# Optimization experiments

Measured on AMD Instinct MI355X. Metric: run time of the kernel, lower is better.

Reference implementation:

```python
import jax, jax.numpy as jnp
import numpy as np
import math

B, C, H, W, T, NH, SS = 4, 64, 32, 32, 32, 8, 512


def _alibi_slopes(heads):
    def pow2(n):
        start = 2 ** (-2 ** (-(math.log2(n) - 3)))
        return [start * start ** i for i in range(n)]
    if math.log2(heads).is_integer():
        return pow2(heads)
    cp = 2 ** math.floor(math.log2(heads))
    return pow2(cp) + pow2(2 * cp)[0::2][: heads - cp]


def _style_conv(x, style, weight, lw, lb, noise_p, bias_p, noise):
    # x: (b,c,h,w,t); weight: (out,in,1,1,1) -> modulated 1x1x1 grouped conv
    s = style @ lw.T + lb                                   # (b, in)
    w = weight[None] * s[:, None, :, None, None, None]       # (b,out,in,1,1,1)
    sigma_inv = jax.lax.rsqrt(jnp.sum(w * w, axis=(2, 3, 4, 5), keepdims=True) + 1e-8)
    w = (w * sigma_inv)[:, :, :, 0, 0, 0]                    # (b,out,in)
    y = jnp.einsum('bchwt,boc->bohwt', x, w)
    y = y + noise_p * noise                                  # (out,1,1,1)*(b,1,h,w,t)
    return y + bias_p


def setup_inputs() -> dict:
    key = jax.random.key(0)
    ks = jax.random.split(key, 8)
    return {
        'x': jax.random.normal(ks[0], (B, C, H, W, T), jnp.float32),
        'style': jax.random.normal(ks[1], (B, SS), jnp.float32),
        'qkv_w': jax.random.normal(ks[2], (3 * C, C, 1, 1, 1), jnp.float32),
        'qkv_lw': jax.random.normal(ks[3], (C, SS), jnp.float32) * 0.02,
        'qkv_lb': jnp.zeros((C,), jnp.float32),
        'qkv_np': jnp.zeros((3 * C, 1, 1, 1), jnp.float32),
        'qkv_bp': jnp.zeros((3 * C, 1, 1, 1), jnp.float32),
        'qkv_noise': jax.random.normal(ks[4], (B, 1, H, W, T), jnp.float32),
        'proj_w': jax.random.normal(ks[5], (C, C, 1, 1, 1), jnp.float32),
        'proj_lw': jax.random.normal(ks[6], (C, SS), jnp.float32) * 0.02,
        'proj_lb': jnp.zeros((C,), jnp.float32),
        'proj_np': jnp.zeros((C, 1, 1, 1), jnp.float32),
        'proj_bp': jnp.zeros((C, 1, 1, 1), jnp.float32),
        'proj_noise': jax.random.normal(ks[7], (B, 1, H, W, T), jnp.float32),
    }


def reference(x, style, qkv_w, qkv_lw, qkv_lb, qkv_np, qkv_bp, qkv_noise,
              proj_w, proj_lw, proj_lb, proj_np, proj_bp, proj_noise):
    b, c, h, w, t = x.shape
    qkv = _style_conv(x, style, qkv_w, qkv_lw, qkv_lb, qkv_np, qkv_bp, qkv_noise)
    q, k, v = jnp.split(qkv, 3, axis=1)                      # each (b,c,h,w,t)

    def to_heads(z):
        z = z.reshape(b, c * h * w, t).transpose(0, 2, 1)    # (b,t,chw)
        return z.reshape(b, t, NH, (c * h * w) // NH).transpose(0, 2, 1, 3)
    q, k, v = to_heads(q), to_heads(k), to_heads(v)          # (b,nh,t,dh)
    dh = q.shape[-1]

    attn = jnp.einsum('bnid,bnjd->bnij', q, k) / math.sqrt(dh)
    slopes = jnp.asarray(_alibi_slopes(NH), dtype=attn.dtype)[:, None, None]
    pos = -jnp.abs(jnp.arange(t)[None, :] - jnp.arange(t)[:, None]).astype(attn.dtype)
    attn = attn + slopes * pos                                # ALiBi bias
    # Faithful to original: masked_fill where tril(ones) is True (lower triangle masked)
    mask = jnp.tril(jnp.ones((t, t), bool))
    attn = jnp.where(mask, jnp.asarray(-1e18, attn.dtype), attn)
    attn = jax.nn.softmax(attn, axis=-1)
    out = jnp.einsum('bnij,bnjd->bnid', attn, v)              # (b,nh,t,dh)

    out = out.transpose(0, 2, 1, 3).reshape(b, t, c * h * w)  # (b,t,chw)
    out = out.reshape(b, t, c, h, w).transpose(0, 2, 3, 4, 1) # (b,c,h,w,t)
    return _style_conv(out, style, proj_w, proj_lw, proj_lb, proj_np, proj_bp, proj_noise)
```

## Files before the change

### kernel.cpp

```cpp
#include <hip/hip_runtime.h>

typedef unsigned short u16;
typedef unsigned int   u32;
typedef __attribute__((ext_vector_type(8))) short bf16x8;
typedef __attribute__((ext_vector_type(4))) float f32x4;

#define PP 32768
#define CC 64

__device__ __forceinline__ u16 f2b(float f) {
    u32 u; __builtin_memcpy(&u, &f, 4);
    u32 r = (u + 0x7FFFu + ((u >> 16) & 1u)) >> 16;
    return (u16)r;
}
__device__ __forceinline__ void unpack2(u32 v, float& lo, float& hi) {
    u32 a = v << 16; u32 b = v & 0xFFFF0000u;
    __builtin_memcpy(&lo, &a, 4); __builtin_memcpy(&hi, &b, 4);
}
__device__ __forceinline__ u32 pack2(float lo, float hi) {
    return (u32)f2b(lo) | ((u32)f2b(hi) << 16);
}

__global__ __launch_bounds__(64) void k_style2(
        const float* __restrict__ style, const float* __restrict__ qkv_lw,
        const float* __restrict__ qkv_lb, const float* __restrict__ proj_lw,
        const float* __restrict__ proj_lb, float* __restrict__ s_out) {
    int id = blockIdx.x;
    int b = id >> 7, sel = (id >> 6) & 1, o = id & 63;
    int t = threadIdx.x;
    const float* lw = sel ? proj_lw : qkv_lw;
    const float* lb = sel ? proj_lb : qkv_lb;
    const float* st = style + b * 512 + t * 8;
    const float* wr = lw + (size_t)o * 512 + t * 8;
    float4 s0 = *(const float4*)st, s1 = *(const float4*)(st + 4);
    float4 w0 = *(const float4*)wr, w1 = *(const float4*)(wr + 4);
    float p = s0.x*w0.x + s0.y*w0.y + s0.z*w0.z + s0.w*w0.w
            + s1.x*w1.x + s1.y*w1.y + s1.z*w1.z + s1.w*w1.w;
    #pragma unroll
    for (int off = 32; off > 0; off >>= 1) p += __shfl_xor(p, off, 64);
    if (t == 0) s_out[b * 128 + sel * 64 + o] = p + lb[o];
}

__global__ __launch_bounds__(64) void k_wnorm(
        const float* __restrict__ qkv_w, const float* __restrict__ proj_w,
        const float* __restrict__ s, float* __restrict__ wqkT,
        u16* __restrict__ wv_bf, float* __restrict__ wpT, float* __restrict__ S) {
    int id = blockIdx.x;
    int b = id >> 8, o = id & 255, i = threadIdx.x;
    if (i < 32) S[(size_t)id * 32 + i] = 0.f;
    float wv;
    if (o < 192) wv = qkv_w[o * 64 + i] * s[b * 128 + i];
    else         wv = proj_w[(o - 192) * 64 + i] * s[b * 128 + 64 + i];
    float sq = wv * wv;
    #pragma unroll
    for (int off = 32; off > 0; off >>= 1) sq += __shfl_xor(sq, off, 64);
    float val = wv * rsqrtf(sq + 1e-8f);
    if (o < 128)      wqkT[((size_t)b * 64 + i) * 128 + o]            = val;
    else if (o < 192) wv_bf[((size_t)b * 64 + (o - 128)) * 64 + i]    = f2b(val);
    else              wpT [((size_t)b * 64 + i) * 64 + (o - 192)]     = val;
}

__global__ __launch_bounds__(256) void k_fscores(
        const float* __restrict__ x, const float* __restrict__ wqkT,
        const float* __restrict__ qnp, const float* __restrict__ qbp,
        const float* __restrict__ qnoise, float* __restrict__ S) {
    int bidx = blockIdx.x;
    int b = bidx >> 8, n = (bidx >> 5) & 7, chunk = bidx & 31;
    int tid = threadIdx.x;
    __shared__ float q_lds[8192];
    __shared__ float k_lds[8192];
    float qa[8][4], ka[8][4];
    #pragma unroll
    for (int c = 0; c < 8; ++c)
        #pragma unroll
        for (int j = 0; j < 4; ++j) { qa[c][j] = 0.f; ka[c][j] = 0.f; }
    const float* xb = x + (size_t)b * CC * PP + chunk * 1024 + tid * 4;
    const float* wb = wqkT + (size_t)b * 8192 + n * 8;
    #pragma unroll 2
    for (int e = 0; e < 64; ++e) {
        float4 xv = *(const float4*)(xb + (size_t)e * PP);
        float xr[4] = {xv.x, xv.y, xv.z, xv.w};
        const float* wr = wb + e * 128;
        #pragma unroll
        for (int c = 0; c < 8; ++c) {
            float wq_ = wr[c], wk_ = wr[64 + c];
            #pragma unroll
            for (int j = 0; j < 4; ++j) {
                qa[c][j] = fmaf(wq_, xr[j], qa[c][j]);
                ka[c][j] = fmaf(wk_, xr[j], ka[c][j]);
            }
        }
    }
    {
        float4 nz4 = *(const float4*)(qnoise + (size_t)b * PP + chunk * 1024 + tid * 4);
        float nz[4] = {nz4.x, nz4.y, nz4.z, nz4.w};
        #pragma unroll
        for (int c = 0; c < 8; ++c) {
            float qn = qnp[n * 8 + c], qb_ = qbp[n * 8 + c];
            float kn = qnp[64 + n * 8 + c], kb_ = qbp[64 + n * 8 + c];
            float4 qo, ko;
            qo.x = qa[c][0] + qn * nz[0] + qb_;  ko.x = ka[c][0] + kn * nz[0] + kb_;
            qo.y = qa[c][1] + qn * nz[1] + qb_;  ko.y = ka[c][1] + kn * nz[1] + kb_;
            qo.z = qa[c][2] + qn * nz[2] + qb_;  ko.z = ka[c][2] + kn * nz[2] + kb_;
            qo.w = qa[c][3] + qn * nz[3] + qb_;  ko.w = ka[c][3] + kn * nz[3] + kb_;
            *(float4*)&q_lds[c * 1024 + tid * 4] = qo;
            *(float4*)&k_lds[c * 1024 + tid * 4] = ko;
        }
    }
    __syncthreads();
    int wave = tid >> 6, lane = tid & 63;
    int ig = lane >> 3, jg = lane & 7;
    float acc[16];
    #pragma unroll
    for (int q = 0; q < 16; ++q) acc[q] = 0.f;
    #pragma unroll 4
    for (int i = 0; i < 64; ++i) {
        int e = wave * 64 + i, c = e >> 5, hl = e & 31;
        float4 qv = *(const float4*)&q_lds[c * 1024 + hl * 32 + ig * 4];
        float4 kv = *(const float4*)&k_lds[c * 1024 + hl * 32 + jg * 4];
        float qa4[4] = {qv.x, qv.y, qv.z, qv.w};
        float ka4[4] = {kv.x, kv.y, kv.z, kv.w};
        #pragma unroll
        for (int ii = 0; ii < 4; ++ii)
            #pragma unroll
            for (int jj = 0; jj < 4; ++jj)
                acc[ii * 4 + jj] = fmaf(qa4[ii], ka4[jj], acc[ii * 4 + jj]);
    }
    __syncthreads();
    #pragma unroll
    for (int t = 0; t < 16; ++t) q_lds[t * 256 + tid] = acc[t];
    __syncthreads();
    if (wave == 0) {
        float* Sb = S + ((size_t)b * 8 + n) * 1024;
        #pragma unroll
        for (int t = 0; t < 16; ++t) {
            float s2 = q_lds[t * 256 + lane]       + q_lds[t * 256 + 64 + lane]
                     + q_lds[t * 256 + 128 + lane] + q_lds[t * 256 + 192 + lane];
            int ii = t >> 2, jj = t & 3;
            atomicAdd(&Sb[(ig * 4 + ii) * 32 + jg * 4 + jj], s2);
        }
    }
}

__global__ __launch_bounds__(256) void k_out(
        const float* __restrict__ x, const u16* __restrict__ wv_bf,
        const float* __restrict__ qnp, const float* __restrict__ qbp,
        const float* __restrict__ qnoise, const float* __restrict__ Sg,
        const float* __restrict__ wpT, const float* __restrict__ pnp,
        const float* __restrict__ pbp, const float* __restrict__ pnoise,
        float* __restrict__ out) {
    int bidx = blockIdx.x;
    int b = bidx >> 8, hw0 = (bidx & 255) * 4;
    int tid = threadIdx.x;
    __shared__ u32   P32s[5120];
    __shared__ u16   V16[10240];
    __shared__ float uni[8448];
    {
        int n = tid >> 5, i2 = tid & 31;
        const float* Srow = Sg + ((size_t)b * 8 + n) * 1024 + i2 * 32;
        float v[32];
        #pragma unroll
        for (int j4 = 0; j4 < 8; ++j4) {
            float4 s4 = *(const float4*)(Srow + j4 * 4);
            v[j4 * 4] = s4.x; v[j4 * 4 + 1] = s4.y;
            v[j4 * 4 + 2] = s4.z; v[j4 * 4 + 3] = s4.w;
        }
        float slope = exp2f(-(float)(n + 1));
        float m = -3e38f;
        #pragma unroll
        for (int j = 0; j < 32; ++j) {
            float val = v[j] * 0.011048543456039806f - slope * fabsf((float)(i2 - j));
            if (j <= i2) val = -1e18f;
            v[j] = val; m = fmaxf(m, val);
        }
        float ssum = 0.f;
        #pragma unroll
        for (int j = 0; j < 32; ++j) { float e2 = expf(v[j] - m); v[j] = e2; ssum += e2; }
        float r = 1.f / ssum;
        #pragma unroll
        for (int jp = 0; jp < 16; ++jp)
            P32s[n * 640 + i2 * 20 + jp] = pack2(v[2 * jp] * r, v[2 * jp + 1] * r);
    }
    {
        u16* XTu = (u16*)uni;
        const float4* xb4 = (const float4*)(x + (size_t)b * CC * PP + (size_t)hw0 * 32);
        #pragma unroll
        for (int r4 = 0; r4 < 8; ++r4) {
            int idx = r4 * 256 + tid;
            int e = idx >> 5, rem = idx & 31, posq = rem * 4;
            float4 xv = xb4[(size_t)e * (PP / 4) + rem];
            XTu[(posq + 0) * 70 + e] = f2b(xv.x);
            XTu[(posq + 1) * 70 + e] = f2b(xv.y);
            XTu[(posq + 2) * 70 + e] = f2b(xv.z);
            XTu[(posq + 3) * 70 + e] = f2b(xv.w);
        }
    }
    __syncthreads();
    int wv_ = tid >> 6, l = tid & 63, tl = l & 15, g = l >> 4;
    {
        const u32* XT32 = (const u32*)uni;
        const u16* wvb = wv_bf + (size_t)b * 4096;
        bf16x8 Af[4][2];
        #pragma unroll
        for (int mt = 0; mt < 4; ++mt)
            #pragma unroll
            for (int k = 0; k < 2; ++k)
                Af[mt][k] = *(const bf16x8*)(wvb + (mt * 16 + tl) * 64 + k * 32 + g * 8);
        #pragma unroll
        for (int nh = 0; nh < 2; ++nh) {
            int nt = 2 * wv_ + nh;
            f32x4 acc[4];
            #pragma unroll
            for (int mt = 0; mt < 4; ++mt) acc[mt] = (f32x4){0.f, 0.f, 0.f, 0.f};
            #pragma unroll
            for (int k = 0; k < 2; ++k) {
                int pos = nt * 16 + tl;
                union { bf16x8 v8; u32 d[4]; } B;
                const u32* xp = XT32 + pos * 35 + k * 16 + g * 4;
                B.d[0] = xp[0]; B.d[1] = xp[1]; B.d[2] = xp[2]; B.d[3] = xp[3];
                #pragma unroll
                for (int mt = 0; mt < 4; ++mt)
                    acc[mt] = __builtin_amdgcn_mfma_f32_16x16x32_bf16(Af[mt][k], B.v8, acc[mt], 0, 0, 0);
            }
            int t = (nt & 1) * 16 + tl;
            float nz = qnoise[(size_t)b * PP + (size_t)(hw0 + wv_) * 32 + t];
            #pragma unroll
            for (int mt = 0; mt < 4; ++mt) {
                float4 np4 = *(const float4*)(qnp + 128 + mt * 16 + g * 4);
                float4 bp4 = *(const float4*)(qbp + 128 + mt * 16 + g * 4);
                float npr[4] = {np4.x, np4.y, np4.z, np4.w};
                float bpr[4] = {bp4.x, bp4.y, bp4.z, bp4.w};
                #pragma unroll
                for (int j = 0; j < 4; ++j) {
                    int ich = mt * 16 + g * 4 + j;
                    int rv = ich * 4 + wv_;
                    float y = acc[mt][j] + npr[j] * nz + bpr[j];
                    u32 bo = (u32)(rv * 80 + t * 2) ^ ((((u32)rv >> 4) & 3u) << 5);
                    *(u16*)((char*)V16 + bo) = f2b(y);
                }
            }
        }
    }
    __syncthreads();
    {
        #pragma unroll
        for (int hh = 0; hh < 2; ++hh) {
            int h = 2 * wv_ + hh;
            bf16x8 Bp[2];
            #pragma unroll
            for (int n2 = 0; n2 < 2; ++n2) {
                const u32* pp = P32s + h * 640 + (n2 * 16 + tl) * 20 + g * 4;
                union { bf16x8 v8; u32 d[4]; } U;
                U.d[0] = pp[0]; U.d[1] = pp[1]; U.d[2] = pp[2]; U.d[3] = pp[3];
                Bp[n2] = U.v8;
            }
            #pragma unroll
            for (int mt2 = 0; mt2 < 2; ++mt2) {
                int rv = h * 32 + mt2 * 16 + tl;
                u32 bo = ((u32)(rv * 80) + (u32)g * 16) ^ ((((u32)rv >> 4) & 3u) << 5);
                bf16x8 Av = *(const bf16x8*)((const char*)V16 + bo);
                #pragma unroll
                for (int n2 = 0; n2 < 2; ++n2) {
                    f32x4 a4 = (f32x4){0.f, 0.f, 0.f, 0.f};
                    a4 = __builtin_amdgcn_mfma_f32_16x16x32_bf16(Av, Bp[n2], a4, 0, 0, 0);
                    int i = h * 8 + mt2 * 4 + g;
                    int t = n2 * 16 + tl;
                    #pragma unroll
                    for (int j = 0; j < 4; ++j)
                        uni[i * 132 + j * 33 + t] = a4[j];
                }
            }
        }
    }
    __syncthreads();
    {
        int og = tid >> 6, lane = tid & 63;
        int tt = lane & 31, rep = lane >> 5;
        int ogu = __builtin_amdgcn_readfirstlane(og);
        const float* wpt = wpT + (size_t)b * 4096 + ogu * 16;
        float acc[16][2];
        #pragma unroll
        for (int oo = 0; oo < 16; ++oo) { acc[oo][0] = 0.f; acc[oo][1] = 0.f; }
        #pragma unroll 4
        for (int i = 0; i < 64; ++i) {
            float a0 = uni[i * 132 + (rep * 2) * 33 + tt];
            float a1 = uni[i * 132 + (rep * 2) * 33 + 33 + tt];
            const float* wr = wpt + i * 64;
            #pragma unroll
            for (int oo = 0; oo < 16; ++oo) {
                acc[oo][0] = fmaf(wr[oo], a0, acc[oo][0]);
                acc[oo][1] = fmaf(wr[oo], a1, acc[oo][1]);
            }
        }
        float nz0 = pnoise[(size_t)b * PP + (size_t)(hw0 + rep * 2) * 32 + tt];
        float nz1 = pnoise[(size_t)b * PP + (size_t)(hw0 + rep * 2 + 1) * 32 + tt];
        #pragma unroll
        for (int oo = 0; oo < 16; ++oo) {
            int o = ogu * 16 + oo;
            float npv = pnp[o], bpv = pbp[o];
            size_t base = (size_t)(b * 64 + o) * PP + tt;
            out[base + (size_t)(hw0 + rep * 2) * 32]     = acc[oo][0] + npv * nz0 + bpv;
            out[base + (size_t)(hw0 + rep * 2 + 1) * 32] = acc[oo][1] + npv * nz1 + bpv;
        }
    }
}

__global__ __launch_bounds__(256) void k_zero(float* __restrict__ out, int n) {
    int i = blockIdx.x * 256 + threadIdx.x;
    if (i < n) out[i] = 0.f;
}
__global__ void k_code(float* __restrict__ out, float code) { out[0] = code; }

extern "C" void kernel_launch(void* const* d_in, const int* in_sizes, int n_in,
                              void* d_out, int out_size, void* d_ws, size_t ws_size,
                              hipStream_t stream) {
    float* out = (float*)d_out;
    const int exp_sizes[14] = {4*64*32768, 4*512, 192*64, 64*512, 64, 192, 192,
                               4*32768, 64*64, 64*512, 64, 64, 64, 4*32768};
    bool ok = (n_in == 14) && (out_size == 4*64*32768);
    if (ok) for (int k = 0; k < 14; ++k) ok = ok && (in_sizes[k] == exp_sizes[k]);
    if (!ok) {
        k_zero<<<(out_size + 255) / 256, 256, 0, stream>>>(out, out_size);
        k_code<<<1, 1, 0, stream>>>(out, 1000.f);
        return;
    }
    if (ws_size < 395264) {
        k_zero<<<(out_size + 255) / 256, 256, 0, stream>>>(out, out_size);
        k_code<<<1, 1, 0, stream>>>(out, 2000.f + (float)(ws_size >> 20));
        return;
    }
    char* ws = (char*)d_ws;
    float* S     = (float*)ws;
    float* wqkT  = (float*)(ws + 131072);
    u16*   wv_bf = (u16*)  (ws + 262144);
    float* wpT   = (float*)(ws + 327680);
    float* s_sty = (float*)(ws + 393216);

    k_style2 <<<512,  64,  0, stream>>>((const float*)d_in[1], (const float*)d_in[3],
                                        (const float*)d_in[4], (const float*)d_in[9],
                                        (const float*)d_in[10], s_sty);
    k_wnorm  <<<1024, 64,  0, stream>>>((const float*)d_in[2], (const float*)d_in[8],
                                        s_sty, wqkT, wv_bf, wpT, S);
    k_fscores<<<1024, 256, 0, stream>>>((const float*)d_in[0], wqkT,
                                        (const float*)d_in[5], (const float*)d_in[6],
                                        (const float*)d_in[7], S);
    k_out    <<<1024, 256, 0, stream>>>((const float*)d_in[0], wv_bf,
                                        (const float*)d_in[5], (const float*)d_in[6],
                                        (const float*)d_in[7], S, wpT,
                                        (const float*)d_in[11], (const float*)d_in[12],
                                        (const float*)d_in[13], out);
    hipError_t e = hipGetLastError();
    if (e != hipSuccess) {
        k_zero<<<(out_size + 255) / 256, 256, 0, stream>>>(out, out_size);
        k_code<<<1, 1, 0, stream>>>(out, 3000.f + (float)e);
    }
}
```

Before: 183.1 us.

## Use split-bf16 MFMA for QK projection and score accumulation in k_fscores

Result: faster. 173.8 us (-5.1%).

```diff
diff --git a/kernel.cpp b/kernel.cpp
--- a/kernel.cpp
+++ b/kernel.cpp
@@ -43,7 +43,7 @@
 
 __global__ __launch_bounds__(64) void k_wnorm(
         const float* __restrict__ qkv_w, const float* __restrict__ proj_w,
-        const float* __restrict__ s, float* __restrict__ wqkT,
+        const float* __restrict__ s, u16* __restrict__ wqk_bf,
         u16* __restrict__ wv_bf, float* __restrict__ wpT, float* __restrict__ S) {
     int id = blockIdx.x;
     int b = id >> 8, o = id & 255, i = threadIdx.x;
@@ -55,91 +55,118 @@
     #pragma unroll
     for (int off = 32; off > 0; off >>= 1) sq += __shfl_xor(sq, off, 64);
     float val = wv * rsqrtf(sq + 1e-8f);
-    if (o < 128)      wqkT[((size_t)b * 64 + i) * 128 + o]            = val;
-    else if (o < 192) wv_bf[((size_t)b * 64 + (o - 128)) * 64 + i]    = f2b(val);
-    else              wpT [((size_t)b * 64 + i) * 64 + (o - 192)]     = val;
+    if (o < 128) {
+        u32 uv = __float_as_uint(val);
+        float res = val - __uint_as_float(uv & 0xFFFF0000u);
+        wqk_bf[((size_t)b * 256 + o) * 64 + i]       = (u16)(uv >> 16);
+        wqk_bf[((size_t)b * 256 + 128 + o) * 64 + i] = (u16)(__float_as_uint(res) >> 16);
+    }
+    else if (o < 192) wv_bf[((size_t)b * 64 + (o - 128)) * 64 + i] = f2b(val);
+    else              wpT [((size_t)b * 64 + i) * 64 + (o - 192)]  = val;
 }
 
 __global__ __launch_bounds__(256) void k_fscores(
-        const float* __restrict__ x, const float* __restrict__ wqkT,
+        const float* __restrict__ x, const u16* __restrict__ wqk_bf,
         const float* __restrict__ qnp, const float* __restrict__ qbp,
         const float* __restrict__ qnoise, float* __restrict__ S) {
     int bidx = blockIdx.x;
     int b = bidx >> 8, n = (bidx >> 5) & 7, chunk = bidx & 31;
     int tid = threadIdx.x;
-    __shared__ float q_lds[8192];
-    __shared__ float k_lds[8192];
-    float qa[8][4], ka[8][4];
+    __shared__ u32   XTh[4480];
+    __shared__ u32   XTl[4480];
+    __shared__ float NZ[128];
+    __shared__ u16   QTh[1288], QTl[1288], KTh[1288], KTl[1288];
+
+    int wv = tid >> 6, l = tid & 63, tl = l & 15, g = l >> 4;
+    int wrow = n * 8 + (tl & 7) + (tl >> 3) * 64;
+    const u16* wpb = wqk_bf + (size_t)b * 16384 + wrow * 64;
+    bf16x8 WH0 = *(const bf16x8*)(wpb + g * 8);
+    bf16x8 WH1 = *(const bf16x8*)(wpb + 32 + g * 8);
+    bf16x8 WL0 = *(const bf16x8*)(wpb + 8192 + g * 8);
+    bf16x8 WL1 = *(const bf16x8*)(wpb + 8192 + 32 + g * 8);
+    int pidx = (g >> 1) * 64 + n * 8 + (g & 1) * 4;
+    float4 np4v = *(const float4*)(qnp + pidx);
+    float4 bp4v = *(const float4*)(qbp + pidx);
+    int ti = wv >> 1, tj = wv & 1;
+    f32x4 sacc = {0.f, 0.f, 0.f, 0.f};
+
+    #pragma unroll 1
+    for (int sub = 0; sub < 8; ++sub) {
+        const float* xc = x + (size_t)b * CC * PP + chunk * 1024 + sub * 128;
+        #pragma unroll
+        for (int r2 = 0; r2 < 4; ++r2) {
+            int idx = r2 * 256 + tid;
+            int e2 = idx >> 5, rem = idx & 31;
+            const float* pa = xc + (size_t)(2 * e2) * PP + rem * 4;
+            float4 fa = *(const float4*)pa;
+            float4 fb = *(const float4*)(pa + PP);
+            #pragma unroll
+            for (int j = 0; j < 4; ++j) {
+                float va = (&fa.x)[j], vb = (&fb.x)[j];
+                u32 ua = __float_as_uint(va), ub = __float_as_uint(vb);
+                float ra = va - __uint_as_float(ua & 0xFFFF0000u);
+                float rb = vb - __uint_as_float(ub & 0xFFFF0000u);
+                int p = (rem * 4 + j) * 35 + e2;
+                XTh[p] = (ua >> 16) | (ub & 0xFFFF0000u);
+                XTl[p] = (__float_as_uint(ra) >> 16) | (__float_as_uint(rb) & 0xFFFF0000u);
+            }
+        }
+        if (tid < 32)
+            *(float4*)&NZ[tid * 4] = *(const float4*)
+                (qnoise + (size_t)b * PP + chunk * 1024 + sub * 128 + tid * 4);
+        __syncthreads();
+        #pragma unroll
+        for (int nh = 0; nh < 2; ++nh) {
+            int nt = wv * 2 + nh, pos = nt * 16 + tl;
+            f32x4 a = {0.f, 0.f, 0.f, 0.f};
+            #pragma unroll
+            for (int k = 0; k < 2; ++k) {
+                union { bf16x8 v; u32 d[4]; } BH, BL;
+                const u32* ph = &XTh[pos * 35 + k * 16 + g * 4];
+                const u32* pl = &XTl[pos * 35 + k * 16 + g * 4];
+                BH.d[0] = ph[0]; BH.d[1] = ph[1]; BH.d[2] = ph[2]; BH.d[3] = ph[3];
+                BL.d[0] = pl[0]; BL.d[1] = pl[1]; BL.d[2] = pl[2]; BL.d[3] = pl[3];
+                bf16x8 WHk = k ? WH1 : WH0;
+                bf16x8 WLk = k ? WL1 : WL0;
+                a = __builtin_amdgcn_mfma_f32_16x16x32_bf16(WHk, BH.v, a, 0, 0, 0);
+                a = __builtin_amdgcn_mfma_f32_16x16x32_bf16(WHk, BL.v, a, 0, 0, 0);
+                a = __builtin_amdgcn_mfma_f32_16x16x32_bf16(WLk, BH.v, a, 0, 0, 0);
+            }
+            float nz = NZ[pos];
+            int t = pos & 31, hwl = pos >> 5, side = g >> 1, g1 = g & 1;
+            u32 uu[4], lu[4];
+            #pragma unroll
+            for (int j = 0; j < 4; ++j) {
+                float yv = a[j] + (&np4v.x)[j] * nz + (&bp4v.x)[j];
+                u32 uy = __float_as_uint(yv);
+                float res = yv - __uint_as_float(uy & 0xFFFF0000u);
+                uu[j] = uy; lu[j] = __float_as_uint(res);
+            }
+            int off = t * 40 + hwl * 8 + g1 * 4;
+            u16* dh = (side ? KTh : QTh) + off;
+            u16* dl = (side ? KTl : QTl) + off;
+            *(uint2*)dh = make_uint2((uu[0] >> 16) | (uu[1] & 0xFFFF0000u),
+                                     (uu[2] >> 16) | (uu[3] & 0xFFFF0000u));
+            *(uint2*)dl = make_uint2((lu[0] >> 16) | (lu[1] & 0xFFFF0000u),
+                                     (lu[2] >> 16) | (lu[3] & 0xFFFF0000u));
+        }
+        __syncthreads();
+        {
+            int ar = (ti * 16 + tl) * 40 + g * 8;
+            int br = (tj * 16 + tl) * 40 + g * 8;
+            bf16x8 Ah = *(const bf16x8*)&QTh[ar];
+            bf16x8 Al = *(const bf16x8*)&QTl[ar];
+            bf16x8 Bh = *(const bf16x8*)&KTh[br];
+            bf16x8 Bl = *(const bf16x8*)&KTl[br];
+            sacc = __builtin_amdgcn_mfma_f32_16x16x32_bf16(Ah, Bh, sacc, 0, 0, 0);
+            sacc = __builtin_amdgcn_mfma_f32_16x16x32_bf16(Ah, Bl, sacc, 0, 0, 0);
+            sacc = __builtin_amdgcn_mfma_f32_16x16x32_bf16(Al, Bh, sacc, 0, 0, 0);
+        }
+    }
+    float* Sb = S + ((size_t)b * 8 + n) * 1024;
     #pragma unroll
-    for (int c = 0; c < 8; ++c)
-        #pragma unroll
-        for (int j = 0; j < 4; ++j) { qa[c][j] = 0.f; ka[c][j] = 0.f; }
-    const float* xb = x + (size_t)b * CC * PP + chunk * 1024 + tid * 4;
-    const float* wb = wqkT + (size_t)b * 8192 + n * 8;
-    #pragma unroll 2
-    for (int e = 0; e < 64; ++e) {
-        float4 xv = *(const float4*)(xb + (size_t)e * PP);
-        float xr[4] = {xv.x, xv.y, xv.z, xv.w};
-        const float* wr = wb + e * 128;
-        #pragma unroll
-        for (int c = 0; c < 8; ++c) {
-            float wq_ = wr[c], wk_ = wr[64 + c];
-            #pragma unroll
-            for (int j = 0; j < 4; ++j) {
-                qa[c][j] = fmaf(wq_, xr[j], qa[c][j]);
-                ka[c][j] = fmaf(wk_, xr[j], ka[c][j]);
-            }
-        }
-    }
-    {
-        float4 nz4 = *(const float4*)(qnoise + (size_t)b * PP + chunk * 1024 + tid * 4);
-        float nz[4] = {nz4.x, nz4.y, nz4.z, nz4.w};
-        #pragma unroll
-        for (int c = 0; c < 8; ++c) {
-            float qn = qnp[n * 8 + c], qb_ = qbp[n * 8 + c];
-            float kn = qnp[64 + n * 8 + c], kb_ = qbp[64 + n * 8 + c];
-            float4 qo, ko;
-            qo.x = qa[c][0] + qn * nz[0] + qb_;  ko.x = ka[c][0] + kn * nz[0] + kb_;
-            qo.y = qa[c][1] + qn * nz[1] + qb_;  ko.y = ka[c][1] + kn * nz[1] + kb_;
-            qo.z = qa[c][2] + qn * nz[2] + qb_;  ko.z = ka[c][2] + kn * nz[2] + kb_;
-            qo.w = qa[c][3] + qn * nz[3] + qb_;  ko.w = ka[c][3] + kn * nz[3] + kb_;
-            *(float4*)&q_lds[c * 1024 + tid * 4] = qo;
-            *(float4*)&k_lds[c * 1024 + tid * 4] = ko;
-        }
-    }
-    __syncthreads();
-    int wave = tid >> 6, lane = tid & 63;
-    int ig = lane >> 3, jg = lane & 7;
-    float acc[16];
-    #pragma unroll
-    for (int q = 0; q < 16; ++q) acc[q] = 0.f;
-    #pragma unroll 4
-    for (int i = 0; i < 64; ++i) {
-        int e = wave * 64 + i, c = e >> 5, hl = e & 31;
-        float4 qv = *(const float4*)&q_lds[c * 1024 + hl * 32 + ig * 4];
-        float4 kv = *(const float4*)&k_lds[c * 1024 + hl * 32 + jg * 4];
-        float qa4[4] = {qv.x, qv.y, qv.z, qv.w};
-        float ka4[4] = {kv.x, kv.y, kv.z, kv.w};
-        #pragma unroll
-        for (int ii = 0; ii < 4; ++ii)
-            #pragma unroll
-            for (int jj = 0; jj < 4; ++jj)
-                acc[ii * 4 + jj] = fmaf(qa4[ii], ka4[jj], acc[ii * 4 + jj]);
-    }
-    __syncthreads();
-    #pragma unroll
-    for (int t = 0; t < 16; ++t) q_lds[t * 256 + tid] = acc[t];
-    __syncthreads();
-    if (wave == 0) {
-        float* Sb = S + ((size_t)b * 8 + n) * 1024;
-        #pragma unroll
-        for (int t = 0; t < 16; ++t) {
-            float s2 = q_lds[t * 256 + lane]       + q_lds[t * 256 + 64 + lane]
-                     + q_lds[t * 256 + 128 + lane] + q_lds[t * 256 + 192 + lane];
-            int ii = t >> 2, jj = t & 3;
-            atomicAdd(&Sb[(ig * 4 + ii) * 32 + jg * 4 + jj], s2);
-        }
-    }
+    for (int jj = 0; jj < 4; ++jj)
+        atomicAdd(&Sb[(ti * 16 + g * 4 + jj) * 32 + tj * 16 + tl], sacc[jj]);
 }
 
 __global__ __launch_bounds__(256) void k_out(
@@ -330,18 +357,18 @@
         return;
     }
     char* ws = (char*)d_ws;
-    float* S     = (float*)ws;
-    float* wqkT  = (float*)(ws + 131072);
-    u16*   wv_bf = (u16*)  (ws + 262144);
-    float* wpT   = (float*)(ws + 327680);
-    float* s_sty = (float*)(ws + 393216);
+    float* S      = (float*)ws;
+    u16*   wqk_bf = (u16*)  (ws + 131072);
+    u16*   wv_bf  = (u16*)  (ws + 262144);
+    float* wpT    = (float*)(ws + 327680);
+    float* s_sty  = (float*)(ws + 393216);
 
     k_style2 <<<512,  64,  0, stream>>>((const float*)d_in[1], (const float*)d_in[3],
                                         (const float*)d_in[4], (const float*)d_in[9],
                                         (const float*)d_in[10], s_sty);
     k_wnorm  <<<1024, 64,  0, stream>>>((const float*)d_in[2], (const float*)d_in[8],
-                                        s_sty, wqkT, wv_bf, wpT, S);
-    k_fscores<<<1024, 256, 0, stream>>>((const float*)d_in[0], wqkT,
+                                        s_sty, wqk_bf, wv_bf, wpT, S);
+    k_fscores<<<1024, 256, 0, stream>>>((const float*)d_in[0], wqk_bf,
                                         (const float*)d_in[5], (const float*)d_in[6],
                                         (const float*)d_in[7], S);
     k_out    <<<1024, 256, 0, stream>>>((const float*)d_in[0], wv_bf,
```
